# Optimization experiments

Measured on AMD Instinct MI355X. Metric: run time of the kernel, lower is better.

The kernel has to match this reference:

```python
import jax, jax.numpy as jnp
import numpy as np

# class -> task group (from class_groups), and per-class distance thresholds
GROUP = jnp.array([0, 1, 1, 2, 2, 3, 4, 4, 5, 5], dtype=jnp.int32)
HIGH_T = jnp.array([2.0, 2.5, 2.5, 3.5, 2.5, 0.5, 1.0, 1.0, 0.5, 0.5], dtype=jnp.float32)
MED_T = jnp.array([4.0, 4.0, 4.0, 4.0, 4.0, 2.5, 2.5, 2.5, 2.0, 2.0], dtype=jnp.float32)
NEAR_THRESH = 30.0
FAR_THRESH = 50.0
FP_THRESH = 4.0


def setup_inputs() -> dict:
    key = jax.random.key(0)
    ks = jax.random.split(key, 7)
    B, R, G = 8, 4096, 512
    roi_xy = jax.random.uniform(ks[0], (B, R, 2), minval=-54.0, maxval=54.0)
    roi_rest = jax.random.normal(ks[1], (B, R, 7))
    rois = jnp.concatenate([roi_xy, roi_rest], axis=-1)            # (B,R,9)
    roi_scores = jax.random.uniform(ks[2], (B, R))                  # (B,R)
    roi_labels = jax.random.randint(ks[3], (B, R), 0, 10)           # (B,R)
    gt_xy = jax.random.uniform(ks[4], (B, G, 2), minval=-54.0, maxval=54.0)
    gt_rest = jax.random.normal(ks[5], (B, G, 7))
    gt_cls = jax.random.randint(ks[6], (B, G), 0, 10).astype(jnp.float32)
    gt_boxes_and_cls = jnp.concatenate([gt_xy, gt_rest, gt_cls[..., None]], axis=-1)  # (B,G,10)
    return {"rois": rois, "roi_scores": roi_scores, "gt_boxes_and_cls": gt_boxes_and_cls,
            "roi_labels": roi_labels, "batch_size": B}


def _forward(rois, roi_scores, gt, roi_labels):
    B, R, _ = rois.shape
    G = gt.shape[1]
    f32 = rois.dtype
    valid_roi = rois.sum(-1) != 0                                   # (B,R) padding filter
    valid_gt = gt.sum(-1) != 0                                      # (B,G)
    gt_cls = jnp.clip(gt[..., -1].astype(jnp.int32), 0, 9)         # (B,G)
    roi_grp = GROUP[jnp.clip(roi_labels.astype(jnp.int32), 0, 9)]  # (B,R)
    gt_grp = GROUP[gt_cls]                                          # (B,G)

    # BEV center distances (B,R,G) using x,y only
    diff = rois[:, :, None, :2] - gt[:, None, :, :2]
    d = jnp.sqrt((diff ** 2).sum(-1))

    same = roi_grp[:, :, None] == gt_grp[:, None, :]
    pv = valid_roi[:, :, None] & valid_gt[:, None, :]
    ht = HIGH_T[gt_cls][:, None, :]                                 # (B,1,G)->bcast
    mt = MED_T[gt_cls][:, None, :]
    high_mask = (d <= ht) & same & pv                               # (B,R,G)
    med_mask = (d > ht) & (d <= mt) & same & pv

    NEG = jnp.asarray(-1e9, f32)
    has_high = high_mask.any(axis=1)                                # (B,G)
    has_med = med_mask.any(axis=1)

    # best-scoring high ROI per GT
    hi = jnp.argmax(jnp.where(high_mask, roi_scores[:, :, None], NEG), axis=1)  # (B,G)
    high_roi = jnp.take_along_axis(rois, hi[:, :, None], axis=1)    # (B,G,9)
    high_score = jnp.take_along_axis(roi_scores, hi, axis=1)        # (B,G)
    refined_score = jnp.minimum((1.2 + high_score) / 2.0, 1.0)

    # best-scoring medium ROI per GT (used only when no high match)
    mi = jnp.argmax(jnp.where(med_mask, roi_scores[:, :, None], NEG), axis=1)
    med_roi = jnp.take_along_axis(rois, mi[:, :, None], axis=1)
    med_score = jnp.take_along_axis(roi_scores, mi, axis=1)
    sel_med = (~has_high) & has_med

    # unmatched GTs bucketed by range from ego (near/medium/far)
    unmatched = valid_gt & (~has_high) & (~has_med)
    rng = jnp.sqrt(gt[..., 0] ** 2 + gt[..., 1] ** 2)
    near = unmatched & (rng < NEAR_THRESH)
    far = unmatched & (rng > FAR_THRESH)
    midb = unmatched & (~near) & (~far)

    # false-positive ROIs: min distance to any valid GT > 4.0
    dmin = jnp.min(jnp.where(valid_gt[:, None, :], d, jnp.inf), axis=2)  # (B,R)
    fp = valid_roi & (dmin > FP_THRESH)

    hv = has_high.astype(f32)[..., None]
    mv = sel_med.astype(f32)[..., None]
    matched = (has_high | sel_med).astype(f32)[..., None]
    onehot = jnp.stack([near, midb, far], axis=-1).astype(f32)      # (B,G,3)
    outG = jnp.concatenate([
        high_roi * hv, (refined_score[..., None]) * hv, hv,
        med_roi * mv, (med_score[..., None]) * mv, mv,
        gt * matched, onehot], axis=-1)                             # (B,G,35)
    fpf = fp.astype(f32)
    outR = jnp.stack([fpf * roi_scores, fpf], axis=-1)              # (B,R,2)
    return jnp.concatenate([outG.reshape(B, -1), outR.reshape(B, -1)], axis=1)


def reference(rois, roi_scores, gt_boxes_and_cls, roi_labels, batch_size):
    return _forward(rois, roi_scores, gt_boxes_and_cls, roi_labels)
```

## Files before the change

kernel.cpp:

```cpp
#include <hip/hip_runtime.h>
#include <stdint.h>

#define NB 8
#define NR 4096
#define NG 512
#define OUTG 35
#define PER_B (NG*OUTG + NR*2)

__constant__ int   c_GROUP[10] = {0,1,1,2,2,3,4,4,5,5};
__constant__ float c_HIGH[10]  = {2.0f,2.5f,2.5f,3.5f,2.5f,0.5f,1.0f,1.0f,0.5f,0.5f};
__constant__ float c_MED[10]   = {4.0f,4.0f,4.0f,4.0f,4.0f,2.5f,2.5f,2.5f,2.0f,2.0f};

__device__ __forceinline__ float sqrt_le_bound(float t) {
  float B = t * t;
  while (sqrtf(__uint_as_float(__float_as_uint(B) + 1u)) <= t)
    B = __uint_as_float(__float_as_uint(B) + 1u);
  return B;
}

__device__ __forceinline__ void write_gt_row(
    float* __restrict__ og, const float gv[10], bool gvalid,
    unsigned long long uh, unsigned long long um,
    const float* __restrict__ rois_b) {
  bool has_high = (uh != 0ull);
  bool has_med  = (um != 0ull);
  bool sel_med  = (!has_high) && has_med;
  bool matched  = has_high || has_med;
  int   hi  = NR - 1 - (int)(unsigned int)(uh & 0xffffffffull);
  int   mi  = NR - 1 - (int)(unsigned int)(um & 0xffffffffull);
  float hsc = __uint_as_float((unsigned int)(uh >> 32) - 1u);
  float msc = __uint_as_float((unsigned int)(um >> 32) - 1u);
  const float* hr = rois_b + (size_t)(has_high ? hi : 0) * 9;
  const float* mr = rois_b + (size_t)(sel_med ? mi : 0) * 9;
  #pragma unroll
  for (int k = 0; k < 9; ++k) og[k] = has_high ? hr[k] : 0.0f;
  og[9]  = has_high ? fminf((1.2f + hsc) * 0.5f, 1.0f) : 0.0f;
  og[10] = has_high ? 1.0f : 0.0f;
  #pragma unroll
  for (int k = 0; k < 9; ++k) og[11 + k] = sel_med ? mr[k] : 0.0f;
  og[20] = sel_med ? msc : 0.0f;
  og[21] = sel_med ? 1.0f : 0.0f;
  #pragma unroll
  for (int k = 0; k < 10; ++k) og[22 + k] = matched ? gv[k] : 0.0f;
  bool unmatched = gvalid && !has_high && !has_med;
  float rng  = sqrtf(__fmul_rn(gv[0], gv[0]) + __fmul_rn(gv[1], gv[1]));
  bool nearb = unmatched && (rng < 30.0f);
  bool farb  = unmatched && (rng > 50.0f);
  bool midb  = unmatched && !nearb && !farb;
  og[32] = nearb ? 1.0f : 0.0f;
  og[33] = midb  ? 1.0f : 0.0f;
  og[34] = farb  ? 1.0f : 0.0f;
}

__global__ __launch_bounds__(512) void fused_kernel(
    const float* __restrict__ rois,
    const float* __restrict__ scores,
    const float* __restrict__ gt,
    const int*   __restrict__ labels,
    float* __restrict__ out) {
  __shared__ float4 sroi[NR];
  __shared__ float2 sgt[NG];

  int tid = threadIdx.x;
  int bid = blockIdx.x;
  int b   = bid >> 5;
  int sub = bid & 31;

  const float* rois_b = rois   + (size_t)b * NR * 9;
  const float* sc_b   = scores + (size_t)b * NR;
  const int*   lab_b  = labels + (size_t)b * NR;
  const float* gt_b   = gt     + (size_t)b * NG * 10;

  #pragma unroll 4
  for (int k = 0; k < 8; ++k) {
    int r = tid + k * 512;
    const float* rr = rois_b + (size_t)r * 9;
    float s = rr[0];
    #pragma unroll
    for (int j = 1; j < 9; ++j) s += rr[j];
    bool valid = (s != 0.0f);
    int lab = min(max(lab_b[r], 0), 9);
    float w = valid ? (float)c_GROUP[lab] : -1.0f;
    sroi[r] = make_float4(rr[0], rr[1], sc_b[r], w);
  }
  {
    const float* gr = gt_b + (size_t)tid * 10;
    float s = gr[0];
    #pragma unroll
    for (int j = 1; j < 10; ++j) s += gr[j];
    bool valid = (s != 0.0f);
    sgt[tid] = make_float2(valid ? gr[0] : 1e30f, valid ? gr[1] : 1e30f);
  }
  __syncthreads();

  int wave = tid >> 6;
  int lane = tid & 63;
  int g0   = sub * 16 + wave * 2;

  float gv0[10], gv1[10];
  {
    const float* gp = gt_b + (size_t)g0 * 10;
    #pragma unroll
    for (int k = 0; k < 10; ++k) gv0[k] = gp[k];
    #pragma unroll
    for (int k = 0; k < 10; ++k) gv1[k] = gp[10 + k];
  }
  float s0 = gv0[0], s1 = gv1[0];
  #pragma unroll
  for (int k = 1; k < 10; ++k) { s0 += gv0[k]; s1 += gv1[k]; }
  bool gvalid0 = (s0 != 0.0f), gvalid1 = (s1 != 0.0f);

  int cls0 = min(max((int)gv0[9], 0), 9);
  int cls1 = min(max((int)gv1[9], 0), 9);
  float Bh0 = sqrt_le_bound(c_HIGH[cls0]);
  float Bm0 = sqrt_le_bound(c_MED[cls0]);
  float Bh1 = sqrt_le_bound(c_HIGH[cls1]);
  float Bm1 = sqrt_le_bound(c_MED[cls1]);
  float gw0 = gvalid0 ? (float)c_GROUP[cls0] : -2.0f;
  float gw1 = gvalid1 ? (float)c_GROUP[cls1] : -2.0f;
  float gx0 = gv0[0], gy0 = gv0[1];
  float gx1 = gv1[0], gy1 = gv1[1];

  unsigned long long uh0 = 0ull, um0 = 0ull, uh1 = 0ull, um1 = 0ull;
  #pragma unroll 4
  for (int r = lane; r < NR; r += 64) {
    float4 p = sroi[r];
    unsigned long long key =
        ((unsigned long long)(__float_as_uint(p.z) + 1u) << 32) |
        (unsigned int)(NR - 1 - r);
    {
      float dx = p.x - gx0, dy = p.y - gy0;
      float d2 = __fmul_rn(dx, dx) + __fmul_rn(dy, dy);
      bool mm = (p.w == gw0) && (d2 <= Bm0);
      bool hh = mm && (d2 <= Bh0);
      bool ee = mm && !(d2 <= Bh0);
      if (hh && key > uh0) uh0 = key;
      if (ee && key > um0) um0 = key;
    }
    {
      float dx = p.x - gx1, dy = p.y - gy1;
      float d2 = __fmul_rn(dx, dx) + __fmul_rn(dy, dy);
      bool mm = (p.w == gw1) && (d2 <= Bm1);
      bool hh = mm && (d2 <= Bh1);
      bool ee = mm && !(d2 <= Bh1);
      if (hh && key > uh1) uh1 = key;
      if (ee && key > um1) um1 = key;
    }
  }
  #pragma unroll
  for (int off = 32; off > 0; off >>= 1) {
    unsigned long long t;
    t = __shfl_xor(uh0, off, 64); if (t > uh0) uh0 = t;
    t = __shfl_xor(um0, off, 64); if (t > um0) um0 = t;
    t = __shfl_xor(uh1, off, 64); if (t > uh1) uh1 = t;
    t = __shfl_xor(um1, off, 64); if (t > um1) um1 = t;
  }

  float* outb = out + (size_t)b * PER_B;
  if (lane == 0) {
    write_gt_row(outb + (size_t)g0 * OUTG, gv0, gvalid0, uh0, um0, rois_b);
  } else if (lane == 1) {
    write_gt_row(outb + (size_t)(g0 + 1) * OUTG, gv1, gvalid1, uh1, um1, rois_b);
  }

  {
    int rl = tid >> 2;
    int q  = tid & 3;
    int r  = sub * 128 + rl;
    float4 p = sroi[r];
    float m2 = __builtin_inff();
    #pragma unroll 4
    for (int jj = 0; jj < 128; ++jj) {
      int j = q * 128 + ((jj + q * 4) & 127);
      float2 qq = sgt[j];
      float dx = p.x - qq.x, dy = p.y - qq.y;
      float d2 = __fmul_rn(dx, dx) + __fmul_rn(dy, dy);
      m2 = fminf(m2, d2);
    }
    float t;
    t = __shfl_xor(m2, 1, 64); m2 = fminf(m2, t);
    t = __shfl_xor(m2, 2, 64); m2 = fminf(m2, t);
    if (q == 0) {
      bool fp = (p.w >= 0.0f) && (sqrtf(m2) > 4.0f);
      float* orow = out + (size_t)b * PER_B + NG * OUTG + (size_t)r * 2;
      orow[0] = fp ? p.z : 0.0f;
      orow[1] = fp ? 1.0f : 0.0f;
    }
  }
}

extern "C" void kernel_launch(void* const* d_in, const int* in_sizes, int n_in,
                              void* d_out, int out_size, void* d_ws, size_t ws_size,
                              hipStream_t stream) {
  const float* rois   = (const float*)d_in[0];
  const float* scores = (const float*)d_in[1];
  const float* gt     = (const float*)d_in[2];
  const int*   labels = (const int*)d_in[3];
  float* out = (float*)d_out;
  (void)d_ws; (void)ws_size;

  fused_kernel<<<NB * 32, 512, 0, stream>>>(rois, scores, gt, labels, out);
}
```

Baseline: 92.68 us.

## Split block into GT-matching and FP waves, merge high/med keys into one

Instead of every thread doing both matching and the false-positive scan, the first four waves now match four GT boxes each and the other four waves handle the FP test with two threads per ROI. The high and medium argmax trackers are packed into a single 64-bit key whose top bit marks a high match, which halves the comparisons and shuffle reductions. The FP test replaces the running minimum and sqrt with an 'any distance within bound' flag and reads GT centres as float4 pairs. The two wave groups now run different code with different amounts of work, so the slower group sets the block's duration.

```diff
diff --git a/kernel.cpp b/kernel.cpp
--- a/kernel.cpp
+++ b/kernel.cpp
@@ -20,29 +20,24 @@
 
 __device__ __forceinline__ void write_gt_row(
     float* __restrict__ og, const float gv[10], bool gvalid,
-    unsigned long long uh, unsigned long long um,
-    const float* __restrict__ rois_b) {
-  bool has_high = (uh != 0ull);
-  bool has_med  = (um != 0ull);
-  bool sel_med  = (!has_high) && has_med;
-  bool matched  = has_high || has_med;
-  int   hi  = NR - 1 - (int)(unsigned int)(uh & 0xffffffffull);
-  int   mi  = NR - 1 - (int)(unsigned int)(um & 0xffffffffull);
-  float hsc = __uint_as_float((unsigned int)(uh >> 32) - 1u);
-  float msc = __uint_as_float((unsigned int)(um >> 32) - 1u);
-  const float* hr = rois_b + (size_t)(has_high ? hi : 0) * 9;
-  const float* mr = rois_b + (size_t)(sel_med ? mi : 0) * 9;
+    unsigned long long key, const float* __restrict__ rois_b) {
+  bool has_match = (key != 0ull);
+  bool has_high  = (key >> 44) != 0ull;
+  bool sel_med   = has_match && !has_high;
+  int   idx = NR - 1 - (int)(key & 0xFFFull);
+  float sc  = __uint_as_float((unsigned int)((key >> 12) & 0xFFFFFFFFull) - 1u);
+  const float* wr = rois_b + (size_t)(has_match ? idx : 0) * 9;
   #pragma unroll
-  for (int k = 0; k < 9; ++k) og[k] = has_high ? hr[k] : 0.0f;
-  og[9]  = has_high ? fminf((1.2f + hsc) * 0.5f, 1.0f) : 0.0f;
+  for (int k = 0; k < 9; ++k) og[k] = has_high ? wr[k] : 0.0f;
+  og[9]  = has_high ? fminf((1.2f + sc) * 0.5f, 1.0f) : 0.0f;
   og[10] = has_high ? 1.0f : 0.0f;
   #pragma unroll
-  for (int k = 0; k < 9; ++k) og[11 + k] = sel_med ? mr[k] : 0.0f;
-  og[20] = sel_med ? msc : 0.0f;
+  for (int k = 0; k < 9; ++k) og[11 + k] = sel_med ? wr[k] : 0.0f;
+  og[20] = sel_med ? sc : 0.0f;
   og[21] = sel_med ? 1.0f : 0.0f;
   #pragma unroll
-  for (int k = 0; k < 10; ++k) og[22 + k] = matched ? gv[k] : 0.0f;
-  bool unmatched = gvalid && !has_high && !has_med;
+  for (int k = 0; k < 10; ++k) og[22 + k] = has_match ? gv[k] : 0.0f;
+  bool unmatched = gvalid && !has_match;
   float rng  = sqrtf(__fmul_rn(gv[0], gv[0]) + __fmul_rn(gv[1], gv[1]));
   bool nearb = unmatched && (rng < 30.0f);
   bool farb  = unmatched && (rng > 50.0f);
@@ -59,7 +54,7 @@
     const int*   __restrict__ labels,
     float* __restrict__ out) {
   __shared__ float4 sroi[NR];
-  __shared__ float2 sgt[NG];
+  __shared__ __align__(16) float2 sgt[NG];
 
   int tid = threadIdx.x;
   int bid = blockIdx.x;
@@ -93,95 +88,114 @@
   }
   __syncthreads();
 
-  int wave = tid >> 6;
-  int lane = tid & 63;
-  int g0   = sub * 16 + wave * 2;
-
-  float gv0[10], gv1[10];
-  {
-    const float* gp = gt_b + (size_t)g0 * 10;
+  if (tid < 256) {
+    int wave = tid >> 6;
+    int lane = tid & 63;
+    int g0   = sub * 16 + wave * 4;
+
+    float gx[4], gy[4], gw[4], Bh[4], Bm[4];
+    {
+      const float* gp = gt_b + (size_t)g0 * 10;
+      #pragma unroll
+      for (int i = 0; i < 4; ++i) {
+        float gv[10];
+        #pragma unroll
+        for (int k = 0; k < 10; ++k) gv[k] = gp[i * 10 + k];
+        float s = gv[0];
+        #pragma unroll
+        for (int k = 1; k < 10; ++k) s += gv[k];
+        bool gvalid = (s != 0.0f);
+        int cls = min(max((int)gv[9], 0), 9);
+        gx[i] = gv[0];
+        gy[i] = gv[1];
+        Bh[i] = sqrt_le_bound(c_HIGH[cls]);
+        Bm[i] = sqrt_le_bound(c_MED[cls]);
+        gw[i] = gvalid ? (float)c_GROUP[cls] : -2.0f;
+      }
+    }
+
+    unsigned long long best0 = 0ull, best1 = 0ull, best2 = 0ull, best3 = 0ull;
+    #pragma unroll 4
+    for (int r = lane; r < NR; r += 64) {
+      float4 p = sroi[r];
+      unsigned int sc1 = __float_as_uint(p.z) + 1u;
+      unsigned long long base =
+          ((unsigned long long)sc1 << 12) | (unsigned int)(NR - 1 - r);
+      {
+        float dx = p.x - gx[0], dy = p.y - gy[0];
+        float d2 = __fmul_rn(dx, dx) + __fmul_rn(dy, dy);
+        bool mm = (p.w == gw[0]) && (d2 <= Bm[0]);
+        unsigned long long key = base | ((d2 <= Bh[0]) ? (1ull << 44) : 0ull);
+        if (mm && key > best0) best0 = key;
+      }
+      {
+        float dx = p.x - gx[1], dy = p.y - gy[1];
+        float d2 = __fmul_rn(dx, dx) + __fmul_rn(dy, dy);
+        bool mm = (p.w == gw[1]) && (d2 <= Bm[1]);
+        unsigned long long key = base | ((d2 <= Bh[1]) ? (1ull << 44) : 0ull);
+        if (mm && key > best1) best1 = key;
+      }
+      {
+        float dx = p.x - gx[2], dy = p.y - gy[2];
+        float d2 = __fmul_rn(dx, dx) + __fmul_rn(dy, dy);
+        bool mm = (p.w == gw[2]) && (d2 <= Bm[2]);
+        unsigned long long key = base | ((d2 <= Bh[2]) ? (1ull << 44) : 0ull);
+        if (mm && key > best2) best2 = key;
+      }
+      {
+        float dx = p.x - gx[3], dy = p.y - gy[3];
+        float d2 = __fmul_rn(dx, dx) + __fmul_rn(dy, dy);
+        bool mm = (p.w == gw[3]) && (d2 <= Bm[3]);
+        unsigned long long key = base | ((d2 <= Bh[3]) ? (1ull << 44) : 0ull);
+        if (mm && key > best3) best3 = key;
+      }
+    }
     #pragma unroll
-    for (int k = 0; k < 10; ++k) gv0[k] = gp[k];
-    #pragma unroll
-    for (int k = 0; k < 10; ++k) gv1[k] = gp[10 + k];
-  }
-  float s0 = gv0[0], s1 = gv1[0];
-  #pragma unroll
-  for (int k = 1; k < 10; ++k) { s0 += gv0[k]; s1 += gv1[k]; }
-  bool gvalid0 = (s0 != 0.0f), gvalid1 = (s1 != 0.0f);
-
-  int cls0 = min(max((int)gv0[9], 0), 9);
-  int cls1 = min(max((int)gv1[9], 0), 9);
-  float Bh0 = sqrt_le_bound(c_HIGH[cls0]);
-  float Bm0 = sqrt_le_bound(c_MED[cls0]);
-  float Bh1 = sqrt_le_bound(c_HIGH[cls1]);
-  float Bm1 = sqrt_le_bound(c_MED[cls1]);
-  float gw0 = gvalid0 ? (float)c_GROUP[cls0] : -2.0f;
-  float gw1 = gvalid1 ? (float)c_GROUP[cls1] : -2.0f;
-  float gx0 = gv0[0], gy0 = gv0[1];
-  float gx1 = gv1[0], gy1 = gv1[1];
-
-  unsigned long long uh0 = 0ull, um0 = 0ull, uh1 = 0ull, um1 = 0ull;
-  #pragma unroll 4
-  for (int r = lane; r < NR; r += 64) {
-    float4 p = sroi[r];
-    unsigned long long key =
-        ((unsigned long long)(__float_as_uint(p.z) + 1u) << 32) |
-        (unsigned int)(NR - 1 - r);
-    {
-      float dx = p.x - gx0, dy = p.y - gy0;
-      float d2 = __fmul_rn(dx, dx) + __fmul_rn(dy, dy);
-      bool mm = (p.w == gw0) && (d2 <= Bm0);
-      bool hh = mm && (d2 <= Bh0);
-      bool ee = mm && !(d2 <= Bh0);
-      if (hh && key > uh0) uh0 = key;
-      if (ee && key > um0) um0 = key;
-    }
-    {
-      float dx = p.x - gx1, dy = p.y - gy1;
-      float d2 = __fmul_rn(dx, dx) + __fmul_rn(dy, dy);
-      bool mm = (p.w == gw1) && (d2 <= Bm1);
-      bool hh = mm && (d2 <= Bh1);
-      bool ee = mm && !(d2 <= Bh1);
-      if (hh && key > uh1) uh1 = key;
-      if (ee && key > um1) um1 = key;
-    }
-  }
-  #pragma unroll
-  for (int off = 32; off > 0; off >>= 1) {
-    unsigned long long t;
-    t = __shfl_xor(uh0, off, 64); if (t > uh0) uh0 = t;
-    t = __shfl_xor(um0, off, 64); if (t > um0) um0 = t;
-    t = __shfl_xor(uh1, off, 64); if (t > uh1) uh1 = t;
-    t = __shfl_xor(um1, off, 64); if (t > um1) um1 = t;
-  }
-
-  float* outb = out + (size_t)b * PER_B;
-  if (lane == 0) {
-    write_gt_row(outb + (size_t)g0 * OUTG, gv0, gvalid0, uh0, um0, rois_b);
-  } else if (lane == 1) {
-    write_gt_row(outb + (size_t)(g0 + 1) * OUTG, gv1, gvalid1, uh1, um1, rois_b);
-  }
-
-  {
-    int rl = tid >> 2;
-    int q  = tid & 3;
+    for (int off = 32; off > 0; off >>= 1) {
+      unsigned long long t;
+      t = __shfl_xor(best0, off, 64); if (t > best0) best0 = t;
+      t = __shfl_xor(best1, off, 64); if (t > best1) best1 = t;
+      t = __shfl_xor(best2, off, 64); if (t > best2) best2 = t;
+      t = __shfl_xor(best3, off, 64); if (t > best3) best3 = t;
+    }
+
+    if (lane < 4) {
+      unsigned long long key = (lane == 0) ? best0
+                             : (lane == 1) ? best1
+                             : (lane == 2) ? best2 : best3;
+      int g = g0 + lane;
+      const float* gr = gt_b + (size_t)g * 10;
+      float gv[10];
+      #pragma unroll
+      for (int k = 0; k < 10; ++k) gv[k] = gr[k];
+      float s = gv[0];
+      #pragma unroll
+      for (int k = 1; k < 10; ++k) s += gv[k];
+      bool gvalid = (s != 0.0f);
+      float* og = out + (size_t)b * PER_B + (size_t)g * OUTG;
+      write_gt_row(og, gv, gvalid, key, rois_b);
+    }
+  } else {
+    int t  = tid - 256;
+    int rl = t >> 1;
+    int q  = t & 1;
     int r  = sub * 128 + rl;
     float4 p = sroi[r];
-    float m2 = __builtin_inff();
+    float B4 = sqrt_le_bound(4.0f);
+    const float4* sgt4 = (const float4*)sgt;
+    int fnd = 0;
     #pragma unroll 4
-    for (int jj = 0; jj < 128; ++jj) {
-      int j = q * 128 + ((jj + q * 4) & 127);
-      float2 qq = sgt[j];
-      float dx = p.x - qq.x, dy = p.y - qq.y;
-      float d2 = __fmul_rn(dx, dx) + __fmul_rn(dy, dy);
-      m2 = fminf(m2, d2);
-    }
-    float t;
-    t = __shfl_xor(m2, 1, 64); m2 = fminf(m2, t);
-    t = __shfl_xor(m2, 2, 64); m2 = fminf(m2, t);
+    for (int j = 0; j < 128; ++j) {
+      float4 v = sgt4[q * 128 + j];
+      float dxa = p.x - v.x, dya = p.y - v.y;
+      float d2a = __fmul_rn(dxa, dxa) + __fmul_rn(dya, dya);
+      float dxb = p.x - v.z, dyb = p.y - v.w;
+      float d2b = __fmul_rn(dxb, dxb) + __fmul_rn(dyb, dyb);
+      fnd |= (int)(d2a <= B4) | (int)(d2b <= B4);
+    }
+    fnd |= __shfl_xor(fnd, 1, 64);
     if (q == 0) {
-      bool fp = (p.w >= 0.0f) && (sqrtf(m2) > 4.0f);
+      bool fp = (p.w >= 0.0f) && !fnd;
       float* orow = out + (size_t)b * PER_B + NG * OUTG + (size_t)r * 2;
       orow[0] = fp ? p.z : 0.0f;
       orow[1] = fp ? 1.0f : 0.0f;
```

After: 80.26 us. 13.4% less time.
